# Kernel optimization log

Hardware: AMD Instinct MI355X
Metric: run time of the kernel (lower is better)

Reference implementation:

```python
import jax, jax.numpy as jnp
import numpy as np

N = 50000
E = 800000
F_IN = 128
HID = 128
OUT = 64
EPS = 1e-5


def gcn_conv(x, src, dst, deg_inv_sqrt, W, b):
    # h = x @ W  (dense transform first, like PyG GCNConv)
    h = x @ W  # [N, F_out]
    norm = deg_inv_sqrt[src] * deg_inv_sqrt[dst]  # [E+N] (self-loops included)
    msgs = norm[:, None] * h[src]  # gather + scale, [E+N, F_out]
    out = jax.ops.segment_sum(msgs, dst, num_segments=N)  # scatter-add to targets
    return out + b


def setup_inputs() -> dict:
    key = jax.random.key(0)
    ks = jax.random.split(key, 9)
    x = jax.random.normal(ks[0], (N, F_IN), dtype=jnp.float32)
    edge_index = jax.random.randint(ks[1], (2, E), 0, N, dtype=jnp.int64)
    s = 1.0 / np.sqrt(F_IN)
    W1 = jax.random.uniform(ks[2], (F_IN, HID), jnp.float32, -s, s)
    b1 = jnp.zeros((HID,), jnp.float32)
    sh = 1.0 / np.sqrt(HID)
    Wmu = jax.random.uniform(ks[3], (HID, OUT), jnp.float32, -sh, sh)
    bmu = jnp.zeros((OUT,), jnp.float32)
    Wlv = jax.random.uniform(ks[4], (HID, OUT), jnp.float32, -sh, sh)
    blv = jnp.zeros((OUT,), jnp.float32)
    gamma = jnp.ones((HID,), jnp.float32)
    beta = jnp.zeros((HID,), jnp.float32)
    return {"x": x, "edge_index": edge_index, "W1": W1, "b1": b1,
            "gamma": gamma, "beta": beta, "Wmu": Wmu, "bmu": bmu,
            "Wlv": Wlv, "blv": blv}


def reference(x, edge_index, W1, b1, gamma, beta, Wmu, bmu, Wlv, blv):
    # Add self-loops (GCNConv default) and compute symmetric normalization once.
    loop = jnp.arange(N, dtype=edge_index.dtype)
    src = jnp.concatenate([edge_index[0], loop])
    dst = jnp.concatenate([edge_index[1], loop])
    deg = jax.ops.segment_sum(jnp.ones_like(dst, dtype=x.dtype), dst, num_segments=N)
    deg_inv_sqrt = jnp.where(deg > 0, jax.lax.rsqrt(deg), 0.0)

    h = jax.nn.relu(gcn_conv(x, src, dst, deg_inv_sqrt, W1, b1))
    # per-node LayerNorm over feature dim
    mean = jnp.mean(h, axis=-1, keepdims=True)
    var = jnp.var(h, axis=-1, keepdims=True)
    h = (h - mean) * jax.lax.rsqrt(var + EPS) * gamma + beta

    mu = gcn_conv(h, src, dst, deg_inv_sqrt, Wmu, bmu)
    logvar = gcn_conv(h, src, dst, deg_inv_sqrt, Wlv, blv)
    return mu, logvar
```

## Files before the change

kernel.cpp:

```cpp
#include <hip/hip_runtime.h>

#define NN 50000
#define EE 800000
#define FF 128
#define OO 64
#define EPSF 1e-5f
#define SCB 196
#define EBLK 3125
#define GBLK 391

typedef unsigned int uint;
typedef unsigned short ushort;
typedef __attribute__((ext_vector_type(8))) short short8;
typedef __attribute__((ext_vector_type(4))) float f32x4;
typedef __attribute__((ext_vector_type(4))) uint uintx4;
typedef __attribute__((ext_vector_type(4))) float floatx4;

__device__ __forceinline__ float bflo(uint v) { return __uint_as_float(v << 16); }
__device__ __forceinline__ float bfhi(uint v) { return __uint_as_float(v & 0xFFFF0000u); }
__device__ __forceinline__ uint f2bf(float f) {
  uint b = __float_as_uint(f);
  return (b + 0x7FFFu + ((b >> 16) & 1u)) >> 16;
}
__device__ __forceinline__ uint pack2(float x, float y) { return f2bf(x) | (f2bf(y) << 16); }

__device__ __forceinline__ int eidx(const void* ei, long long pos, int f64) {
  if (f64) return (int)((const long long*)ei)[pos];
  return ((const int*)ei)[pos];
}

__global__ void k_init(const void* ei, int* flag, int* cnt) {
  int i = blockIdx.x * 256 + threadIdx.x;
  if (i < NN) cnt[i] = 0;
  if (i == 0) {
    const int* p = (const int*)ei;
    int any = 0;
    for (int j = 1; j < 128; j += 2) any |= p[j];
    *flag = (any == 0) ? 1 : 0;
  }
}

__device__ __forceinline__ int wt_idx(int c, int k) {
  return c * 128 + (k ^ ((c & 7) << 3));
}

__global__ __launch_bounds__(256) void k_deg_gemm1(
    const void* ei, const int* __restrict__ flag,
    int* __restrict__ cnt, int* __restrict__ rank,
    const float* __restrict__ X, const float* __restrict__ W,
    ushort* __restrict__ T) {
  __shared__ ushort Wt[FF * FF];
  if (blockIdx.x < EBLK) {
    int e = blockIdx.x * 256 + threadIdx.x;
    if (e >= EE) return;
    int f64 = *flag;
    int d = eidx(ei, (long long)EE + e, f64);
    rank[e] = atomicAdd(&cnt[d], 1);
    return;
  }
  int gblk = blockIdx.x - EBLK;
  for (int i = threadIdx.x; i < FF * FF; i += 256) {
    int k = i >> 7, c = i & 127;
    Wt[wt_idx(c, k)] = (ushort)f2bf(W[i]);
  }
  __syncthreads();
  int l = threadIdx.x & 63, wv = threadIdx.x >> 6;
  int rbase = gblk * 128 + wv * 32;
  int lr = l & 15, lk = (l >> 4) << 3;
  f32x4 acc[2][8] = {};
#pragma unroll
  for (int kb = 0; kb < 4; ++kb) {
    int kk = kb * 32 + lk;
    short8 a[2];
#pragma unroll
    for (int rt = 0; rt < 2; ++rt) {
      int row = min(rbase + rt * 16 + lr, NN - 1);
      const float4* ap = (const float4*)(X + (size_t)row * FF + kk);
      float4 x0 = ap[0], x1 = ap[1];
      a[rt][0] = (short)f2bf(x0.x); a[rt][1] = (short)f2bf(x0.y);
      a[rt][2] = (short)f2bf(x0.z); a[rt][3] = (short)f2bf(x0.w);
      a[rt][4] = (short)f2bf(x1.x); a[rt][5] = (short)f2bf(x1.y);
      a[rt][6] = (short)f2bf(x1.z); a[rt][7] = (short)f2bf(x1.w);
    }
#pragma unroll
    for (int ct = 0; ct < 8; ++ct) {
      int c = ct * 16 + lr;
      short8 b = *(const short8*)&Wt[wt_idx(c, kk)];
      acc[0][ct] = __builtin_amdgcn_mfma_f32_16x16x32_bf16(a[0], b, acc[0][ct], 0, 0, 0);
      acc[1][ct] = __builtin_amdgcn_mfma_f32_16x16x32_bf16(a[1], b, acc[1][ct], 0, 0, 0);
    }
  }
  int rl = (l >> 4) * 4;
#pragma unroll
  for (int rt = 0; rt < 2; ++rt)
#pragma unroll
    for (int reg = 0; reg < 4; ++reg) {
      int row = rbase + rt * 16 + rl + reg;
      if (row < NN) {
#pragma unroll
        for (int ct = 0; ct < 8; ++ct)
          T[(size_t)row * FF + ct * 16 + lr] = (ushort)f2bf(acc[rt][ct][reg]);
      }
    }
}

__global__ __launch_bounds__(256) void k_dis_part(const int* __restrict__ cnt,
                                                  float* __restrict__ dis,
                                                  int* __restrict__ bsum) {
  int i = blockIdx.x * 256 + threadIdx.x;
  int v = (i < NN) ? cnt[i] : 0;
  if (i < NN) dis[i] = rsqrtf((float)(v + 1));
  int s = v;
#pragma unroll
  for (int m = 1; m < 64; m <<= 1) s += __shfl_xor(s, m);
  __shared__ int ws[4];
  if ((threadIdx.x & 63) == 0) ws[threadIdx.x >> 6] = s;
  __syncthreads();
  if (threadIdx.x == 0) bsum[blockIdx.x] = ws[0] + ws[1] + ws[2] + ws[3];
}

__global__ __launch_bounds__(256) void k_scan_all(const int* __restrict__ cnt,
                                                  const int* __restrict__ bsum,
                                                  int* __restrict__ rowptr) {
  __shared__ int s[256];
  __shared__ int vv[256];
  __shared__ int wsum[4];
  int tid = threadIdx.x, blk = blockIdx.x;
  int v = (tid < SCB) ? bsum[tid] : 0;
  s[tid] = v;
  vv[tid] = v;
  __syncthreads();
  for (int off = 1; off < 256; off <<= 1) {
    int t = (tid >= off) ? s[tid - off] : 0;
    __syncthreads();
    s[tid] += t;
    __syncthreads();
  }
  if (blk == 0 && tid == 255) rowptr[NN] = s[255];
  int boff = s[blk] - vv[blk];
  int i = blk * 256 + tid;
  int c = (i < NN) ? cnt[i] : 0;
  int lane = tid & 63, wid = tid >> 6;
  int inc = c;
#pragma unroll
  for (int off = 1; off < 64; off <<= 1) {
    int t = __shfl_up(inc, off);
    if (lane >= off) inc += t;
  }
  if (lane == 63) wsum[wid] = inc;
  __syncthreads();
  int wadd = 0;
  for (int wj = 0; wj < wid; ++wj) wadd += wsum[wj];
  int exc = inc - c + wadd + boff;
  if (i < NN) rowptr[i] = exc;
}

__global__ void k_scatter(const void* ei, const int* __restrict__ flag,
                          const float* __restrict__ dis,
                          const int* __restrict__ rowptr,
                          const int* __restrict__ rank,
                          int2* __restrict__ cw) {
  int e = blockIdx.x * 256 + threadIdx.x;
  if (e >= EE) return;
  int f64 = *flag;
  int s = eidx(ei, e, f64);
  int d = eidx(ei, (long long)EE + e, f64);
  int p = rowptr[d] + rank[e];
  int2 v;
  v.x = s;
  v.y = __float_as_int(dis[s] * dis[d]);
  cw[p] = v;
}

__global__ __launch_bounds__(256) void k_gemmHW(const ushort* __restrict__ A,
                                                const float* __restrict__ Wmu,
                                                const float* __restrict__ Wlv,
                                                ushort* __restrict__ T) {
  __shared__ ushort Wt[FF * FF];
  for (int i = threadIdx.x; i < FF * FF; i += 256) {
    int k = i >> 7, c = i & 127;
    float v = (c < OO) ? Wmu[k * OO + c] : Wlv[k * OO + (c - OO)];
    Wt[wt_idx(c, k)] = (ushort)f2bf(v);
  }
  __syncthreads();
  int l = threadIdx.x & 63, wv = threadIdx.x >> 6;
  int rbase = blockIdx.x * 128 + wv * 32;
  int lr = l & 15, lk = (l >> 4) << 3;
  f32x4 acc[2][8] = {};
#pragma unroll
  for (int kb = 0; kb < 4; ++kb) {
    int kk = kb * 32 + lk;
    short8 a[2];
#pragma unroll
    for (int rt = 0; rt < 2; ++rt) {
      int row = min(rbase + rt * 16 + lr, NN - 1);
      a[rt] = *(const short8*)(A + (size_t)row * FF + kk);
    }
#pragma unroll
    for (int ct = 0; ct < 8; ++ct) {
      int c = ct * 16 + lr;
      short8 b = *(const short8*)&Wt[wt_idx(c, kk)];
      acc[0][ct] = __builtin_amdgcn_mfma_f32_16x16x32_bf16(a[0], b, acc[0][ct], 0, 0, 0);
      acc[1][ct] = __builtin_amdgcn_mfma_f32_16x16x32_bf16(a[1], b, acc[1][ct], 0, 0, 0);
    }
  }
  int rl = (l >> 4) * 4;
#pragma unroll
  for (int rt = 0; rt < 2; ++rt)
#pragma unroll
    for (int reg = 0; reg < 4; ++reg) {
      int row = rbase + rt * 16 + rl + reg;
      if (row < NN) {
#pragma unroll
        for (int ct = 0; ct < 8; ++ct)
          T[(size_t)row * FF + ct * 16 + lr] = (ushort)f2bf(acc[rt][ct][reg]);
      }
    }
}

__global__ __launch_bounds__(256) void k_gather_ln(const int* __restrict__ rowptr,
                                                   const int2* __restrict__ cw,
                                                   const float* __restrict__ dis,
                                                   const ushort* __restrict__ feat,
                                                   const float* __restrict__ b1,
                                                   const float* __restrict__ gamma,
                                                   const float* __restrict__ beta,
                                                   ushort* __restrict__ outp) {
  int node = blockIdx.x * 4 + (threadIdx.x >> 6);
  if (node >= NN) return;
  int l = threadIdx.x & 63;
  int g = l >> 4;
  int c16 = l & 15;

  float di = dis[node];
  uint4 vSelf = ((const uint4*)(feat + ((size_t)node << 7)))[c16];

  float acc[8] = {};
  int e0 = rowptr[node], nE = rowptr[node + 1] - e0;
  int base = 0;
  for (; base + 8 <= nE; base += 8) {
    int2 cA = cw[e0 + base + g];
    int2 cB = cw[e0 + base + 4 + g];
    uint4 vA = ((const uint4*)(feat + ((size_t)cA.x << 7)))[c16];
    uint4 vB = ((const uint4*)(feat + ((size_t)cB.x << 7)))[c16];
    float wA = __int_as_float(cA.y), wB = __int_as_float(cB.y);
    acc[0] = fmaf(wA, bflo(vA.x), acc[0]); acc[1] = fmaf(wA, bfhi(vA.x), acc[1]);
    acc[2] = fmaf(wA, bflo(vA.y), acc[2]); acc[3] = fmaf(wA, bfhi(vA.y), acc[3]);
    acc[4] = fmaf(wA, bflo(vA.z), acc[4]); acc[5] = fmaf(wA, bfhi(vA.z), acc[5]);
    acc[6] = fmaf(wA, bflo(vA.w), acc[6]); acc[7] = fmaf(wA, bfhi(vA.w), acc[7]);
    acc[0] = fmaf(wB, bflo(vB.x), acc[0]); acc[1] = fmaf(wB, bfhi(vB.x), acc[1]);
    acc[2] = fmaf(wB, bflo(vB.y), acc[2]); acc[3] = fmaf(wB, bfhi(vB.y), acc[3]);
    acc[4] = fmaf(wB, bflo(vB.z), acc[4]); acc[5] = fmaf(wB, bfhi(vB.z), acc[5]);
    acc[6] = fmaf(wB, bflo(vB.w), acc[6]); acc[7] = fmaf(wB, bfhi(vB.w), acc[7]);
  }
#pragma unroll
  for (int t = 0; t < 2; ++t) {
    int idx = base + t * 4 + g;
    if (idx < nE) {
      int2 c0 = cw[e0 + idx];
      uint4 v = ((const uint4*)(feat + ((size_t)c0.x << 7)))[c16];
      float w0 = __int_as_float(c0.y);
      acc[0] = fmaf(w0, bflo(v.x), acc[0]); acc[1] = fmaf(w0, bfhi(v.x), acc[1]);
      acc[2] = fmaf(w0, bflo(v.y), acc[2]); acc[3] = fmaf(w0, bfhi(v.y), acc[3]);
      acc[4] = fmaf(w0, bflo(v.z), acc[4]); acc[5] = fmaf(w0, bfhi(v.z), acc[5]);
      acc[6] = fmaf(w0, bflo(v.w), acc[6]); acc[7] = fmaf(w0, bfhi(v.w), acc[7]);
    }
  }
#pragma unroll
  for (int j = 0; j < 8; ++j) {
    acc[j] += __shfl_xor(acc[j], 16);
    acc[j] += __shfl_xor(acc[j], 32);
  }
  {
    float sw = di * di;
    acc[0] = fmaf(sw, bflo(vSelf.x), acc[0]); acc[1] = fmaf(sw, bfhi(vSelf.x), acc[1]);
    acc[2] = fmaf(sw, bflo(vSelf.y), acc[2]); acc[3] = fmaf(sw, bfhi(vSelf.y), acc[3]);
    acc[4] = fmaf(sw, bflo(vSelf.z), acc[4]); acc[5] = fmaf(sw, bfhi(vSelf.z), acc[5]);
    acc[6] = fmaf(sw, bflo(vSelf.w), acc[6]); acc[7] = fmaf(sw, bfhi(vSelf.w), acc[7]);
  }
  int cOff = c16 * 8;
  float4 ba = *(const float4*)&b1[cOff];
  float4 bb = *(const float4*)&b1[cOff + 4];
  float a[8];
  a[0] = fmaxf(acc[0] + ba.x, 0.f); a[1] = fmaxf(acc[1] + ba.y, 0.f);
  a[2] = fmaxf(acc[2] + ba.z, 0.f); a[3] = fmaxf(acc[3] + ba.w, 0.f);
  a[4] = fmaxf(acc[4] + bb.x, 0.f); a[5] = fmaxf(acc[5] + bb.y, 0.f);
  a[6] = fmaxf(acc[6] + bb.z, 0.f); a[7] = fmaxf(acc[7] + bb.w, 0.f);
  float s = 0.f, sq = 0.f;
#pragma unroll
  for (int j = 0; j < 8; ++j) { s += a[j]; sq += a[j] * a[j]; }
#pragma unroll
  for (int m = 1; m < 16; m <<= 1) {
    s += __shfl_xor(s, m);
    sq += __shfl_xor(sq, m);
  }
  float mean = s * (1.f / 128.f);
  float var = sq * (1.f / 128.f) - mean * mean;
  float rstd = rsqrtf(var + EPSF);
  float4 ga = *(const float4*)&gamma[cOff];
  float4 gb = *(const float4*)&gamma[cOff + 4];
  float4 ea = *(const float4*)&beta[cOff];
  float4 eb = *(const float4*)&beta[cOff + 4];
  float o[8];
  o[0] = (a[0] - mean) * rstd * ga.x + ea.x; o[1] = (a[1] - mean) * rstd * ga.y + ea.y;
  o[2] = (a[2] - mean) * rstd * ga.z + ea.z; o[3] = (a[3] - mean) * rstd * ga.w + ea.w;
  o[4] = (a[4] - mean) * rstd * gb.x + eb.x; o[5] = (a[5] - mean) * rstd * gb.y + eb.y;
  o[6] = (a[6] - mean) * rstd * gb.z + eb.z; o[7] = (a[7] - mean) * rstd * gb.w + eb.w;
  if (g == 0) {
    uintx4 p;
    p.x = pack2(o[0], o[1]); p.y = pack2(o[2], o[3]);
    p.z = pack2(o[4], o[5]); p.w = pack2(o[6], o[7]);
    __builtin_nontemporal_store(p, (uintx4*)(outp + ((size_t)node << 7)) + c16);
  }
}

__global__ __launch_bounds__(256) void k_gather_out(const int* __restrict__ rowptr,
                                                    const int2* __restrict__ cw,
                                                    const float* __restrict__ dis,
                                                    const ushort* __restrict__ feat,
                                                    const float* __restrict__ bmu,
                                                    const float* __restrict__ blv,
                                                    float* __restrict__ out) {
  int node = blockIdx.x * 4 + (threadIdx.x >> 6);
  if (node >= NN) return;
  int l = threadIdx.x & 63;
  int g = l >> 4;
  int c16 = l & 15;

  float di = dis[node];
  uint4 vSelf = ((const uint4*)(feat + ((size_t)node << 7)))[c16];

  float acc[8] = {};
  int e0 = rowptr[node], nE = rowptr[node + 1] - e0;
  int base = 0;
  for (; base + 8 <= nE; base += 8) {
    int2 cA = cw[e0 + base + g];
    int2 cB = cw[e0 + base + 4 + g];
    uint4 vA = ((const uint4*)(feat + ((size_t)cA.x << 7)))[c16];
    uint4 vB = ((const uint4*)(feat + ((size_t)cB.x << 7)))[c16];
    float wA = __int_as_float(cA.y), wB = __int_as_float(cB.y);
    acc[0] = fmaf(wA, bflo(vA.x), acc[0]); acc[1] = fmaf(wA, bfhi(vA.x), acc[1]);
    acc[2] = fmaf(wA, bflo(vA.y), acc[2]); acc[3] = fmaf(wA, bfhi(vA.y), acc[3]);
    acc[4] = fmaf(wA, bflo(vA.z), acc[4]); acc[5] = fmaf(wA, bfhi(vA.z), acc[5]);
    acc[6] = fmaf(wA, bflo(vA.w), acc[6]); acc[7] = fmaf(wA, bfhi(vA.w), acc[7]);
    acc[0] = fmaf(wB, bflo(vB.x), acc[0]); acc[1] = fmaf(wB, bfhi(vB.x), acc[1]);
    acc[2] = fmaf(wB, bflo(vB.y), acc[2]); acc[3] = fmaf(wB, bfhi(vB.y), acc[3]);
    acc[4] = fmaf(wB, bflo(vB.z), acc[4]); acc[5] = fmaf(wB, bfhi(vB.z), acc[5]);
    acc[6] = fmaf(wB, bflo(vB.w), acc[6]); acc[7] = fmaf(wB, bfhi(vB.w), acc[7]);
  }
#pragma unroll
  for (int t = 0; t < 2; ++t) {
    int idx = base + t * 4 + g;
    if (idx < nE) {
      int2 c0 = cw[e0 + idx];
      uint4 v = ((const uint4*)(feat + ((size_t)c0.x << 7)))[c16];
      float w0 = __int_as_float(c0.y);
      acc[0] = fmaf(w0, bflo(v.x), acc[0]); acc[1] = fmaf(w0, bfhi(v.x), acc[1]);
      acc[2] = fmaf(w0, bflo(v.y), acc[2]); acc[3] = fmaf(w0, bfhi(v.y), acc[3]);
      acc[4] = fmaf(w0, bflo(v.z), acc[4]); acc[5] = fmaf(w0, bfhi(v.z), acc[5]);
      acc[6] = fmaf(w0, bflo(v.w), acc[6]); acc[7] = fmaf(w0, bfhi(v.w), acc[7]);
    }
  }
#pragma unroll
  for (int j = 0; j < 8; ++j) {
    acc[j] += __shfl_xor(acc[j], 16);
    acc[j] += __shfl_xor(acc[j], 32);
  }
  {
    float sw = di * di;
    acc[0] = fmaf(sw, bflo(vSelf.x), acc[0]); acc[1] = fmaf(sw, bfhi(vSelf.x), acc[1]);
    acc[2] = fmaf(sw, bflo(vSelf.y), acc[2]); acc[3] = fmaf(sw, bfhi(vSelf.y), acc[3]);
    acc[4] = fmaf(sw, bflo(vSelf.z), acc[4]); acc[5] = fmaf(sw, bfhi(vSelf.z), acc[5]);
    acc[6] = fmaf(sw, bflo(vSelf.w), acc[6]); acc[7] = fmaf(sw, bfhi(vSelf.w), acc[7]);
  }
  if (g == 0) {
    const float* bsrc = (c16 < 8) ? (bmu + c16 * 8) : (blv + (c16 - 8) * 8);
    float* osrc = (c16 < 8) ? (out + (size_t)node * OO + c16 * 8)
                            : (out + (size_t)NN * OO + (size_t)node * OO + (c16 - 8) * 8);
    float4 b0 = *(const float4*)bsrc;
    float4 b1 = *(const float4*)(bsrc + 4);
    floatx4 o0 = { acc[0] + b0.x, acc[1] + b0.y, acc[2] + b0.z, acc[3] + b0.w };
    floatx4 o1 = { acc[4] + b1.x, acc[5] + b1.y, acc[6] + b1.z, acc[7] + b1.w };
    __builtin_nontemporal_store(o0, (floatx4*)osrc);
    __builtin_nontemporal_store(o1, (floatx4*)(osrc + 4));
  }
}

extern "C" void kernel_launch(void* const* d_in, const int* in_sizes, int n_in,
                              void* d_out, int out_size, void* d_ws, size_t ws_size,
                              hipStream_t stream) {
  const float* x     = (const float*)d_in[0];
  const void*  ei    = d_in[1];
  const float* W1    = (const float*)d_in[2];
  const float* b1    = (const float*)d_in[3];
  const float* gamma = (const float*)d_in[4];
  const float* beta  = (const float*)d_in[5];
  const float* Wmu   = (const float*)d_in[6];
  const float* bmu   = (const float*)d_in[7];
  const float* Wlv   = (const float*)d_in[8];
  const float* blv   = (const float*)d_in[9];
  float* out = (float*)d_out;

  int*   flag   = (int*)d_ws;
  int*   cnt    = flag + 64;
  int*   rowptr = cnt + NN;
  float* dis    = (float*)(rowptr + (NN + 16));
  int*   bsum   = (int*)(dis + NN);
  int*   rank   = bsum + 256;
  size_t off32  = (size_t)(64 + NN + (NN + 16) + NN + 256 + EE);
  off32 = (off32 + 63) & ~(size_t)63;
  int2*  cw     = (int2*)((int*)d_ws + off32);
  ushort* t  = (ushort*)(cw + EE);
  ushort* h  = t + (size_t)NN * FF;
  ushort* hw = h + (size_t)NN * FF;

  k_init<<<SCB, 256, 0, stream>>>(ei, flag, cnt);
  k_deg_gemm1<<<EBLK + GBLK, 256, 0, stream>>>(ei, flag, cnt, rank, x, W1, t);
  k_dis_part<<<SCB, 256, 0, stream>>>(cnt, dis, bsum);
  k_scan_all<<<SCB, 256, 0, stream>>>(cnt, bsum, rowptr);
  k_scatter<<<EBLK, 256, 0, stream>>>(ei, flag, dis, rowptr, rank, cw);

  k_gather_ln<<<(NN + 3) / 4, 256, 0, stream>>>(rowptr, cw, dis, t, b1, gamma, beta, h);
  k_gemmHW<<<GBLK, 256, 0, stream>>>(h, Wmu, Wlv, hw);
  k_gather_out<<<(NN + 3) / 4, 256, 0, stream>>>(rowptr, cw, dis, hw, bmu, blv, out);
}
```

Before: 166.0 us.

## Co-schedule layer-1 GEMM with edge scatter, drop init kernel and flag

Moves the first dense GEMM out of the degree-counting kernel and into the scatter kernel, so the GEMM blocks run alongside the CSR scatter rather than the atomic degree counting. Replaces the init kernel with hipMemsetAsync and detects the int64 index format per wave with a ballot instead of a global flag. Also swaps the nontemporal store in the LayerNorm kernel for a plain store. Each wave now does a redundant probe load, and the balance of the overlap shifts toward the scatter phase.

```diff
diff --git a/kernel.cpp b/kernel.cpp
--- a/kernel.cpp
+++ b/kernel.cpp
@@ -29,79 +29,18 @@
   return ((const int*)ei)[pos];
 }
 
-__global__ void k_init(const void* ei, int* flag, int* cnt) {
-  int i = blockIdx.x * 256 + threadIdx.x;
-  if (i < NN) cnt[i] = 0;
-  if (i == 0) {
-    const int* p = (const int*)ei;
-    int any = 0;
-    for (int j = 1; j < 128; j += 2) any |= p[j];
-    *flag = (any == 0) ? 1 : 0;
-  }
-}
-
-__device__ __forceinline__ int wt_idx(int c, int k) {
-  return c * 128 + (k ^ ((c & 7) << 3));
-}
-
-__global__ __launch_bounds__(256) void k_deg_gemm1(
-    const void* ei, const int* __restrict__ flag,
-    int* __restrict__ cnt, int* __restrict__ rank,
-    const float* __restrict__ X, const float* __restrict__ W,
-    ushort* __restrict__ T) {
-  __shared__ ushort Wt[FF * FF];
-  if (blockIdx.x < EBLK) {
-    int e = blockIdx.x * 256 + threadIdx.x;
-    if (e >= EE) return;
-    int f64 = *flag;
-    int d = eidx(ei, (long long)EE + e, f64);
-    rank[e] = atomicAdd(&cnt[d], 1);
-    return;
-  }
-  int gblk = blockIdx.x - EBLK;
-  for (int i = threadIdx.x; i < FF * FF; i += 256) {
-    int k = i >> 7, c = i & 127;
-    Wt[wt_idx(c, k)] = (ushort)f2bf(W[i]);
-  }
-  __syncthreads();
-  int l = threadIdx.x & 63, wv = threadIdx.x >> 6;
-  int rbase = gblk * 128 + wv * 32;
-  int lr = l & 15, lk = (l >> 4) << 3;
-  f32x4 acc[2][8] = {};
-#pragma unroll
-  for (int kb = 0; kb < 4; ++kb) {
-    int kk = kb * 32 + lk;
-    short8 a[2];
-#pragma unroll
-    for (int rt = 0; rt < 2; ++rt) {
-      int row = min(rbase + rt * 16 + lr, NN - 1);
-      const float4* ap = (const float4*)(X + (size_t)row * FF + kk);
-      float4 x0 = ap[0], x1 = ap[1];
-      a[rt][0] = (short)f2bf(x0.x); a[rt][1] = (short)f2bf(x0.y);
-      a[rt][2] = (short)f2bf(x0.z); a[rt][3] = (short)f2bf(x0.w);
-      a[rt][4] = (short)f2bf(x1.x); a[rt][5] = (short)f2bf(x1.y);
-      a[rt][6] = (short)f2bf(x1.z); a[rt][7] = (short)f2bf(x1.w);
-    }
-#pragma unroll
-    for (int ct = 0; ct < 8; ++ct) {
-      int c = ct * 16 + lr;
-      short8 b = *(const short8*)&Wt[wt_idx(c, kk)];
-      acc[0][ct] = __builtin_amdgcn_mfma_f32_16x16x32_bf16(a[0], b, acc[0][ct], 0, 0, 0);
-      acc[1][ct] = __builtin_amdgcn_mfma_f32_16x16x32_bf16(a[1], b, acc[1][ct], 0, 0, 0);
-    }
-  }
-  int rl = (l >> 4) * 4;
-#pragma unroll
-  for (int rt = 0; rt < 2; ++rt)
-#pragma unroll
-    for (int reg = 0; reg < 4; ++reg) {
-      int row = rbase + rt * 16 + rl + reg;
-      if (row < NN) {
-#pragma unroll
-        for (int ct = 0; ct < 8; ++ct)
-          T[(size_t)row * FF + ct * 16 + lr] = (ushort)f2bf(acc[rt][ct][reg]);
-      }
-    }
+__device__ __forceinline__ int detect_f64(const void* ei) {
+  int lane = threadIdx.x & 63;
+  int probe = ((const int*)ei)[2 * lane + 1];
+  return __any(probe != 0) ? 0 : 1;
+}
+
+__global__ void k_deg_rank(const void* ei, int* __restrict__ cnt, int* __restrict__ rank) {
+  int e = blockIdx.x * 256 + threadIdx.x;
+  if (e >= EE) return;
+  int f64 = detect_f64(ei);
+  int d = eidx(ei, (long long)EE + e, f64);
+  rank[e] = atomicAdd(&cnt[d], 1);
 }
 
 __global__ __launch_bounds__(256) void k_dis_part(const int* __restrict__ cnt,
@@ -155,21 +94,73 @@
   if (i < NN) rowptr[i] = exc;
 }
 
-__global__ void k_scatter(const void* ei, const int* __restrict__ flag,
-                          const float* __restrict__ dis,
-                          const int* __restrict__ rowptr,
-                          const int* __restrict__ rank,
-                          int2* __restrict__ cw) {
-  int e = blockIdx.x * 256 + threadIdx.x;
-  if (e >= EE) return;
-  int f64 = *flag;
-  int s = eidx(ei, e, f64);
-  int d = eidx(ei, (long long)EE + e, f64);
-  int p = rowptr[d] + rank[e];
-  int2 v;
-  v.x = s;
-  v.y = __float_as_int(dis[s] * dis[d]);
-  cw[p] = v;
+__device__ __forceinline__ int wt_idx(int c, int k) {
+  return c * 128 + (k ^ ((c & 7) << 3));
+}
+
+__global__ __launch_bounds__(256) void k_scatter_gemm1(
+    const void* ei, const float* __restrict__ dis,
+    const int* __restrict__ rowptr, const int* __restrict__ rank,
+    int2* __restrict__ cw,
+    const float* __restrict__ X, const float* __restrict__ W,
+    ushort* __restrict__ T) {
+  __shared__ ushort Wt[FF * FF];
+  if (blockIdx.x >= GBLK) {
+    int e = (blockIdx.x - GBLK) * 256 + threadIdx.x;
+    if (e >= EE) return;
+    int f64 = detect_f64(ei);
+    int s = eidx(ei, e, f64);
+    int d = eidx(ei, (long long)EE + e, f64);
+    int p = rowptr[d] + rank[e];
+    int2 v;
+    v.x = s;
+    v.y = __float_as_int(dis[s] * dis[d]);
+    cw[p] = v;
+    return;
+  }
+  for (int i = threadIdx.x; i < FF * FF; i += 256) {
+    int k = i >> 7, c = i & 127;
+    Wt[wt_idx(c, k)] = (ushort)f2bf(W[i]);
+  }
+  __syncthreads();
+  int l = threadIdx.x & 63, wv = threadIdx.x >> 6;
+  int rbase = blockIdx.x * 128 + wv * 32;
+  int lr = l & 15, lk = (l >> 4) << 3;
+  f32x4 acc[2][8] = {};
+#pragma unroll
+  for (int kb = 0; kb < 4; ++kb) {
+    int kk = kb * 32 + lk;
+    short8 a[2];
+#pragma unroll
+    for (int rt = 0; rt < 2; ++rt) {
+      int row = min(rbase + rt * 16 + lr, NN - 1);
+      const float4* ap = (const float4*)(X + (size_t)row * FF + kk);
+      float4 x0 = ap[0], x1 = ap[1];
+      a[rt][0] = (short)f2bf(x0.x); a[rt][1] = (short)f2bf(x0.y);
+      a[rt][2] = (short)f2bf(x0.z); a[rt][3] = (short)f2bf(x0.w);
+      a[rt][4] = (short)f2bf(x1.x); a[rt][5] = (short)f2bf(x1.y);
+      a[rt][6] = (short)f2bf(x1.z); a[rt][7] = (short)f2bf(x1.w);
+    }
+#pragma unroll
+    for (int ct = 0; ct < 8; ++ct) {
+      int c = ct * 16 + lr;
+      short8 b = *(const short8*)&Wt[wt_idx(c, kk)];
+      acc[0][ct] = __builtin_amdgcn_mfma_f32_16x16x32_bf16(a[0], b, acc[0][ct], 0, 0, 0);
+      acc[1][ct] = __builtin_amdgcn_mfma_f32_16x16x32_bf16(a[1], b, acc[1][ct], 0, 0, 0);
+    }
+  }
+  int rl = (l >> 4) * 4;
+#pragma unroll
+  for (int rt = 0; rt < 2; ++rt)
+#pragma unroll
+    for (int reg = 0; reg < 4; ++reg) {
+      int row = rbase + rt * 16 + rl + reg;
+      if (row < NN) {
+#pragma unroll
+        for (int ct = 0; ct < 8; ++ct)
+          T[(size_t)row * FF + ct * 16 + lr] = (ushort)f2bf(acc[rt][ct][reg]);
+      }
+    }
 }
 
 __global__ __launch_bounds__(256) void k_gemmHW(const ushort* __restrict__ A,
@@ -307,10 +298,10 @@
   o[4] = (a[4] - mean) * rstd * gb.x + eb.x; o[5] = (a[5] - mean) * rstd * gb.y + eb.y;
   o[6] = (a[6] - mean) * rstd * gb.z + eb.z; o[7] = (a[7] - mean) * rstd * gb.w + eb.w;
   if (g == 0) {
-    uintx4 p;
+    uint4 p;
     p.x = pack2(o[0], o[1]); p.y = pack2(o[2], o[3]);
     p.z = pack2(o[4], o[5]); p.w = pack2(o[6], o[7]);
-    __builtin_nontemporal_store(p, (uintx4*)(outp + ((size_t)node << 7)) + c16);
+    ((uint4*)(outp + ((size_t)node << 7)))[c16] = p;
   }
 }
 
@@ -401,24 +392,23 @@
   const float* blv   = (const float*)d_in[9];
   float* out = (float*)d_out;
 
-  int*   flag   = (int*)d_ws;
-  int*   cnt    = flag + 64;
+  int*   cnt    = (int*)d_ws;
   int*   rowptr = cnt + NN;
   float* dis    = (float*)(rowptr + (NN + 16));
   int*   bsum   = (int*)(dis + NN);
   int*   rank   = bsum + 256;
-  size_t off32  = (size_t)(64 + NN + (NN + 16) + NN + 256 + EE);
+  size_t off32  = (size_t)(NN + (NN + 16) + NN + 256 + EE);
   off32 = (off32 + 63) & ~(size_t)63;
   int2*  cw     = (int2*)((int*)d_ws + off32);
   ushort* t  = (ushort*)(cw + EE);
   ushort* h  = t + (size_t)NN * FF;
   ushort* hw = h + (size_t)NN * FF;
 
-  k_init<<<SCB, 256, 0, stream>>>(ei, flag, cnt);
-  k_deg_gemm1<<<EBLK + GBLK, 256, 0, stream>>>(ei, flag, cnt, rank, x, W1, t);
+  hipMemsetAsync(cnt, 0, NN * sizeof(int), stream);
+  k_deg_rank<<<EBLK, 256, 0, stream>>>(ei, cnt, rank);
   k_dis_part<<<SCB, 256, 0, stream>>>(cnt, dis, bsum);
   k_scan_all<<<SCB, 256, 0, stream>>>(cnt, bsum, rowptr);
-  k_scatter<<<EBLK, 256, 0, stream>>>(ei, flag, dis, rowptr, rank, cw);
+  k_scatter_gemm1<<<GBLK + EBLK, 256, 0, stream>>>(ei, dis, rowptr, rank, cw, x, W1, t);
 
   k_gather_ln<<<(NN + 3) / 4, 256, 0, stream>>>(rowptr, cw, dis, t, b1, gamma, beta, h);
   k_gemmHW<<<GBLK, 256, 0, stream>>>(h, Wmu, Wlv, hw);
```

Measured after the change: 155.6 us. 1.07x faster.
